# Performance work log

Hardware: AMD Instinct MI355X
Metric: run time of the kernel (lower is better)

The kernel has to match this reference:

```python
import jax, jax.numpy as jnp
import numpy as np
from jax import lax

H = 256          # hidden_size
VOCAB = 30000
N_OPS = 9
N_COLS = 16
T = 4            # num_time_steps
Q = 64           # question length
N_NUM = 8        # numbers appearing in the question
ROWS = 1_000_000

# operation indices (Neural Programmer, ICLR 2016 op set)
OP_SUM, OP_COUNT, OP_DIFF, OP_GREATER, OP_LESSER, OP_AND, OP_OR, OP_ASSIGN, OP_RESET = range(N_OPS)


def setup_inputs() -> dict:
    key = jax.random.key(0)
    ks = jax.random.split(key, 13)
    s = 0.05
    f32 = jnp.float32
    return {
        "input_question": jax.random.randint(ks[0], (Q,), 0, VOCAB),
        "input_question_numbers": jax.random.randint(ks[1], (N_NUM,), 0, 100),
        "left_word_indices": jax.random.randint(ks[2], (N_NUM,), 0, Q),
        "table": jax.random.normal(ks[3], (ROWS, N_COLS), f32),
        # learned parameters
        "emb": jax.random.normal(ks[4], (VOCAB, H), f32) * s,      # question word embeddings
        "Wx": jax.random.normal(ks[5], (H, H), f32) * s,           # question RNN input weight
        "Wh": jax.random.normal(ks[6], (H, H), f32) * s,           # question RNN recurrent weight
        "W_op": jax.random.normal(ks[7], (H, 2 * H), f32) * s,     # selector (op branch)
        "op_emb": jax.random.normal(ks[8], (N_OPS, H), f32) * s,   # operation embeddings
        "W_col": jax.random.normal(ks[9], (H, 2 * H), f32) * s,    # selector (column branch)
        "col_emb": jax.random.normal(ks[10], (N_COLS, H), f32) * s,# column embeddings
        "W_hist": jax.random.normal(ks[11], (H, 3 * H), f32) * s,  # history RNN
        "U": jax.random.normal(ks[12], (2, H), f32) * s,           # lesser/greater pivot vectors
    }


def reference(input_question, input_question_numbers, left_word_indices, table,
              emb, Wx, Wh, W_op, op_emb, W_col, col_emb, W_hist, U):
    dt = table.dtype
    hid = Wx.shape[0]

    # ---- question RNN (simple tanh RNN) ----
    xs = emb[input_question]                               # [Q, H]
    def step(h, x):
        h2 = jnp.tanh(x @ Wx.T + h @ Wh.T)
        return h2, h2
    q, hs = lax.scan(step, jnp.zeros((hid,), dt), xs)      # q=[H], hs=[Q,H]

    # ---- pivot computation (z_matrix = hidden states left of each number) ----
    z = hs[left_word_indices]                              # [N_NUM, H]
    nums = input_question_numbers.astype(dt)               # [N_NUM]
    l_pivot = jax.nn.softmax(z @ U[0]) @ nums              # scalar
    g_pivot = jax.nn.softmax(z @ U[1]) @ nums              # scalar

    # soft comparison maps (pivots are timestep-independent; compute once)
    sel_l = jax.nn.sigmoid(l_pivot - table)                # [R, C] ~ [table < l_pivot]
    sel_g = jax.nn.sigmoid(table - g_pivot)                # [R, C] ~ [table > g_pivot]

    h_hist = jnp.zeros((hid,), dt)
    scalars = [jnp.zeros((), dt)]
    rs_list = [jnp.ones((table.shape[0],), dt)]
    lookup = jnp.zeros(table.shape, dt)

    for _ in range(T):
        rs1 = rs_list[-1]
        rs2 = rs_list[max(0, len(rs_list) - 2)]
        s1 = scalars[-1]
        s3 = scalars[max(0, len(scalars) - 3)]

        # selector: soft op / column distributions from [question; history]
        qh = jnp.concatenate([q, h_hist])                  # [2H]
        a_op = jax.nn.softmax(op_emb @ jnp.tanh(W_op @ qh))    # [N_OPS]
        a_col = jax.nn.softmax(col_emb @ jnp.tanh(W_col @ qh)) # [N_COLS]

        # row select (soft mixture over ops)
        rs = (a_op[OP_GREATER] * (sel_g @ a_col)
              + a_op[OP_LESSER] * (sel_l @ a_col)
              + a_op[OP_AND] * jnp.minimum(rs1, rs2)
              + a_op[OP_OR] * jnp.maximum(rs1, rs2)
              + a_op[OP_RESET] * jnp.ones_like(rs1)
              + (a_op[OP_SUM] + a_op[OP_COUNT] + a_op[OP_DIFF] + a_op[OP_ASSIGN]) * rs1)

        # scalar answer
        scalar = (a_op[OP_SUM] * jnp.sum(rs1 @ table)
                  + a_op[OP_COUNT] * jnp.sum(rs1)
                  + a_op[OP_DIFF] * (s3 - s1))

        # lookup answer: assign op prints selected rows/columns
        lookup = a_op[OP_ASSIGN] * rs[:, None] * a_col[None, :]

        # history RNN
        c = jnp.concatenate([a_op @ op_emb, a_col @ col_emb, h_hist])  # [3H]
        h_hist = jnp.tanh(W_hist @ c)

        rs_list.append(rs)
        scalars.append(scalar)

    return scalars[-1], lookup
```

## Files before the change

### kernel.cpp

```cpp
#include <hip/hip_runtime.h>
#include <hip/hip_fp16.h>
#include <math.h>

#define HDIM   256
#define QLEN   64
#define NNUM   8
#define NOPS   9
#define NCOLS  16
#define TSTEPS 4


#define WS_LPIV 0
#define WS_GPIV 1
#define WS_ACOL 2
#define WS_AOP  66
#define WS_Q    112
#define WS_PQO  368
#define WS_PQC  624
#define WS_HS   880
#define WS_XP   2928
#define WS_AH   19312
#define WS_BH   21616
#define WS_WH16 25712
#define WS_M16  58480
#define WS_PART 156784
#define NBLK_C  2048
#define PRE2_BLOCKS 409

typedef _Float16 f16x8 __attribute__((ext_vector_type(8)));
typedef _Float16 f16x4 __attribute__((ext_vector_type(4)));
typedef float    f32x4 __attribute__((ext_vector_type(4)));

__device__ __forceinline__ float fast_tanh(float x) {
    return 1.0f - 2.0f / (__expf(2.0f * x) + 1.0f);
}

__global__ void precompute_kernel(const int* __restrict__ q,
                                  const float* __restrict__ emb,
                                  const float* __restrict__ Wx,
                                  const float* __restrict__ Wh,
                                  float* __restrict__ ws) {
    int gid = blockIdx.x * 256 + threadIdx.x;
    if (gid < QLEN * HDIM) {
        int t = gid >> 8, j = gid & 255;
        const float4* x4 = (const float4*)(emb + (size_t)q[t] * HDIM);
        const float4* w4 = (const float4*)(Wx + (size_t)j * HDIM);
        float s = 0.f;
        for (int k = 0; k < HDIM / 4; k++) {
            float4 a = x4[k], b = w4[k];
            s += a.x * b.x + a.y * b.y + a.z * b.z + a.w * b.w;
        }
        ws[WS_XP + t * HDIM + j] = s;
    } else {
        int did = gid - QLEN * HDIM;
        int hidx = did * 2;
        int e = hidx & 7, qr = (hidx >> 3) & 15, quad = (hidx >> 7) & 3;
        int kk = (hidx >> 9) & 7, t = hidx >> 12;
        const float* src = Wh + (size_t)(16 * t + qr) * HDIM + kk * 32 + quad * 8 + e;
        float2 v = *(const float2*)src;
        ((__half2*)(ws + WS_WH16))[did] = __floats2half2_rn(v.x, v.y);
    }
}

__global__ __launch_bounds__(256, 1) void rnn_kernel(
        float* __restrict__ ws,
        const int* __restrict__ lwi,
        const float* __restrict__ W_op,
        const float* __restrict__ W_col,
        const float* __restrict__ W_hist,
        const float* __restrict__ op_emb,
        const float* __restrict__ col_emb,
        const float* __restrict__ table,
        int rows) {
    if (blockIdx.x >= 1 + PRE2_BLOCKS) {
        int wid = blockIdx.x - 1 - PRE2_BLOCKS;
        const f32x4* t4 = (const f32x4*)table;
        long n4 = (long)rows * (NCOLS / 4);
        f32x4 acc = {0.f, 0.f, 0.f, 0.f};
        for (long i = (long)wid * 256 + threadIdx.x; i < n4; i += (long)2048 * 256)
            acc += t4[i];
        asm volatile("" :: "v"(acc));
        return;
    }
    if (blockIdx.x != 0) {
        int gid = (blockIdx.x - 1) * 256 + threadIdx.x;
        if (gid < HDIM * NOPS) {
            int j = gid / NOPS, o = gid % NOPS;
            const float4* w4 = (const float4*)(W_hist + (size_t)j * (3 * HDIM));
            const float4* e4 = (const float4*)(op_emb + (size_t)o * HDIM);
            float s = 0.f;
            for (int k = 0; k < HDIM / 4; k++) {
                float4 a = w4[k], b = e4[k];
                s += a.x * b.x + a.y * b.y + a.z * b.z + a.w * b.w;
            }
            ws[WS_AH + gid] = s;
        } else if (gid < HDIM * NOPS + HDIM * NCOLS) {
            int idx = gid - HDIM * NOPS;
            int j = idx / NCOLS, c = idx % NCOLS;
            const float4* w4 = (const float4*)(W_hist + (size_t)j * (3 * HDIM) + HDIM);
            const float4* e4 = (const float4*)(col_emb + (size_t)c * HDIM);
            float s = 0.f;
            for (int k = 0; k < HDIM / 4; k++) {
                float4 a = w4[k], b = e4[k];
                s += a.x * b.x + a.y * b.y + a.z * b.z + a.w * b.w;
            }
            ws[WS_BH + idx] = s;
        } else if (gid < HDIM * NOPS + HDIM * NCOLS + 98304) {
            int did = gid - (HDIM * NOPS + HDIM * NCOLS);
            int mat = did >> 15;
            int hidx = (did & 32767) * 2;
            int e = hidx & 7, j = (hidx >> 3) & 255, i = hidx >> 11;
            const float* src;
            if (mat == 0)      src = W_op   + (size_t)j * (2 * HDIM) + HDIM     + i * 8 + e;
            else if (mat == 1) src = W_col  + (size_t)j * (2 * HDIM) + HDIM     + i * 8 + e;
            else               src = W_hist + (size_t)j * (3 * HDIM) + 2 * HDIM + i * 8 + e;
            float2 v = *(const float2*)src;
            ((__half2*)(ws + WS_M16))[did] = __floats2half2_rn(v.x, v.y);
        }
        return;
    }

    __shared__ float xpL[QLEN * HDIM];
    __shared__ _Float16 hF[2][HDIM];
    __shared__ unsigned stepmask[QLEN];

    const int tid = threadIdx.x;
    const int wave = tid >> 6, lane = tid & 63;
    const int quad = lane >> 4, qr = lane & 15;
    const int myrow = 64 * wave + 16 * (qr >> 2) + quad * 4 + (qr & 3);

    #pragma unroll
    for (int i = 0; i < 16; i++) {
        int idx = (i * 256 + tid) * 4;
        *(float4*)(xpL + idx) = *(const float4*)(ws + WS_XP + idx);
    }
    if (tid < QLEN) {
        unsigned m = 0;
        #pragma unroll
        for (int i = 0; i < NNUM; i++) m |= (lwi[i] == tid) ? (1u << i) : 0u;
        stepmask[tid] = m;
    }
    const _Float16* wsh = (const _Float16*)(ws + WS_WH16);
    f16x8 aW[4][8];
    #pragma unroll
    for (int r = 0; r < 4; r++)
        #pragma unroll
        for (int kk = 0; kk < 8; kk++)
            aW[r][kk] = *(const f16x8*)(wsh + ((size_t)(((4 * wave + r) * 8 + kk) * 64 + lane)) * 8);
    #pragma unroll
    for (int r = 0; r < 4; r++)
        #pragma unroll
        for (int kk = 0; kk < 8; kk++) {
            f32x4 t = __builtin_bit_cast(f32x4, aW[r][kk]);
            asm volatile("" : "+v"(t));
            aW[r][kk] = __builtin_bit_cast(f16x8, t);
        }
    hF[0][tid] = (_Float16)0.f;
    __syncthreads();

    for (int s = 0; s < QLEN; s++) {
        const _Float16* hb = hF[s & 1];
        f16x8 bfrag[8];
        #pragma unroll
        for (int kk = 0; kk < 8; kk++)
            bfrag[kk] = *(const f16x8*)(hb + kk * 32 + quad * 8);
        f32x4 acc[4], accB[4];
        #pragma unroll
        for (int r = 0; r < 4; r++) {
            acc[r]  = (f32x4){0.f, 0.f, 0.f, 0.f};
            accB[r] = (f32x4){0.f, 0.f, 0.f, 0.f};
        }
        #pragma unroll
        for (int kk = 0; kk < 4; kk++)
            #pragma unroll
            for (int r = 0; r < 4; r++)
                acc[r] = __builtin_amdgcn_mfma_f32_16x16x32_f16(aW[r][kk], bfrag[kk], acc[r], 0, 0, 0);
        #pragma unroll
        for (int kk = 4; kk < 8; kk++)
            #pragma unroll
            for (int r = 0; r < 4; r++)
                accB[r] = __builtin_amdgcn_mfma_f32_16x16x32_f16(aW[r][kk], bfrag[kk], accB[r], 0, 0, 0);
        #pragma unroll
        for (int r = 0; r < 4; r++) acc[r] += accB[r];

        f32x4 t01 = (qr & 4) ? acc[1] : acc[0];
        f32x4 t23 = (qr & 4) ? acc[3] : acc[2];
        f32x4 tt  = (qr & 8) ? t23 : t01;
        float e01 = (qr & 1) ? tt.y : tt.x;
        float e23 = (qr & 1) ? tt.w : tt.z;
        float v   = (qr & 2) ? e23 : e01;

        float h = fast_tanh(v + xpL[s * HDIM + myrow]);
        hF[(s + 1) & 1][myrow] = (_Float16)h;
        unsigned m = stepmask[s];
        while (m) {
            int i = __builtin_ctz(m);
            ws[WS_HS + i * HDIM + myrow] = h;
            m &= m - 1;
        }
        if (s == QLEN - 1) ws[WS_Q + myrow] = h;
        __syncthreads();
    }
}

__global__ void qproj_kernel(const float* __restrict__ W_op,
                             const float* __restrict__ W_col,
                             float* __restrict__ ws) {
    int gid = blockIdx.x * 256 + threadIdx.x;
    int dot = gid >> 5, l = gid & 31;
    int mat = dot >> 8, j = dot & 255;
    const float* w = (mat ? W_col : W_op) + (size_t)j * (2 * HDIM) + l * 8;
    const float* qv = ws + WS_Q + l * 8;
    float4 a0 = *(const float4*)w,        a1 = *(const float4*)(w + 4);
    float4 b0 = *(const float4*)qv,       b1 = *(const float4*)(qv + 4);
    float s = a0.x * b0.x + a0.y * b0.y + a0.z * b0.z + a0.w * b0.w
            + a1.x * b1.x + a1.y * b1.y + a1.z * b1.z + a1.w * b1.w;
    s += __shfl_xor(s, 1); s += __shfl_xor(s, 2); s += __shfl_xor(s, 4);
    s += __shfl_xor(s, 8); s += __shfl_xor(s, 16);
    if (l == 0) ws[(mat ? WS_PQC : WS_PQO) + j] = s;
}

__global__ __launch_bounds__(256) void select_kernel(
        float* __restrict__ ws,
        const float* __restrict__ U,
        const int* __restrict__ nums,
        const float* __restrict__ op_emb,
        const float* __restrict__ col_emb) {
    __shared__ float zu[16];
    __shared__ float hH[HDIM];
    __shared__ float top_op[HDIM], top_col[HDIM], mh[HDIM];
    __shared__ float logits[32];
    __shared__ float aop_s[NOPS], acol_s[NCOLS];

    const int tid = threadIdx.x;

    {
        int g = tid >> 4, l = tid & 15;
        int i = g >> 1, u = g & 1;
        const float* z = ws + WS_HS + i * HDIM + l * 16;
        const float* uu = U + u * HDIM + l * 16;
        float s = 0.f;
        #pragma unroll
        for (int k = 0; k < 4; k++) {
            float4 a = *(const float4*)(z + k * 4), b = *(const float4*)(uu + k * 4);
            s += a.x * b.x + a.y * b.y + a.z * b.z + a.w * b.w;
        }
        s += __shfl_xor(s, 1); s += __shfl_xor(s, 2);
        s += __shfl_xor(s, 4); s += __shfl_xor(s, 8);
        if (l == 0) zu[g] = s;
    }
    if (tid < HDIM) hH[tid] = 0.f;
    __syncthreads();
    if (tid == 0) {
        #pragma unroll
        for (int u = 0; u < 2; u++) {
            float mx = -1e30f;
            for (int i = 0; i < NNUM; i++) mx = fmaxf(mx, zu[i * 2 + u]);
            float se = 0.f, pv = 0.f;
            for (int i = 0; i < NNUM; i++) {
                float e = __expf(zu[i * 2 + u] - mx);
                se += e;
                pv += e * (float)nums[i];
            }
            ws[u] = pv / se;
        }
    }
    __syncthreads();

    const _Float16* wsm = (const _Float16*)(ws + WS_M16);
    const float pqo = ws[WS_PQO + tid];
    const float pqc = ws[WS_PQC + tid];

    for (int t = 0; t < TSTEPS; t++) {
        float so = 0.f, sc = 0.f, sh = 0.f;
        #pragma unroll
        for (int i = 0; i < 32; i++) {
            float4 h0 = *(const float4*)(hH + i * 8);
            float4 h1 = *(const float4*)(hH + i * 8 + 4);
            f16x8 a = *(const f16x8*)(wsm + ((size_t)(0 * 32 + i) * 256 + tid) * 8);
            f16x8 b = *(const f16x8*)(wsm + ((size_t)(1 * 32 + i) * 256 + tid) * 8);
            f16x8 c = *(const f16x8*)(wsm + ((size_t)(2 * 32 + i) * 256 + tid) * 8);
            so += (float)a[0]*h0.x + (float)a[1]*h0.y + (float)a[2]*h0.z + (float)a[3]*h0.w
                + (float)a[4]*h1.x + (float)a[5]*h1.y + (float)a[6]*h1.z + (float)a[7]*h1.w;
            sc += (float)b[0]*h0.x + (float)b[1]*h0.y + (float)b[2]*h0.z + (float)b[3]*h0.w
                + (float)b[4]*h1.x + (float)b[5]*h1.y + (float)b[6]*h1.z + (float)b[7]*h1.w;
            sh += (float)c[0]*h0.x + (float)c[1]*h0.y + (float)c[2]*h0.z + (float)c[3]*h0.w
                + (float)c[4]*h1.x + (float)c[5]*h1.y + (float)c[6]*h1.z + (float)c[7]*h1.w;
        }
        top_op[tid]  = fast_tanh(pqo + so);
        top_col[tid] = fast_tanh(pqc + sc);
        mh[tid] = sh;
        __syncthreads();

        #pragma unroll
        for (int d0 = 0; d0 < 32; d0 += 8) {
            int d = d0 + (tid >> 5), l = tid & 31;
            if (d < 25) {
                float s = 0.f;
                if (d < NOPS) {
                    const float* e = op_emb + (size_t)d * HDIM;
                    #pragma unroll
                    for (int m = 0; m < 8; m++) s += e[l * 8 + m] * top_op[l * 8 + m];
                } else {
                    const float* e = col_emb + (size_t)(d - NOPS) * HDIM;
                    #pragma unroll
                    for (int m = 0; m < 8; m++) s += e[l * 8 + m] * top_col[l * 8 + m];
                }
                s += __shfl_xor(s, 1); s += __shfl_xor(s, 2); s += __shfl_xor(s, 4);
                s += __shfl_xor(s, 8); s += __shfl_xor(s, 16);
                if (l == 0) logits[d] = s;
            }
        }
        __syncthreads();
        if (tid == 0) {
            float mx = -1e30f;
            for (int o = 0; o < NOPS; o++) mx = fmaxf(mx, logits[o]);
            float se = 0.f, e[NOPS];
            for (int o = 0; o < NOPS; o++) { e[o] = __expf(logits[o] - mx); se += e[o]; }
            for (int o = 0; o < NOPS; o++) {
                float a = e[o] / se;
                aop_s[o] = a;
                ws[WS_AOP + t * NOPS + o] = a;
            }
        } else if (tid == 32) {
            float mx = -1e30f;
            for (int c = 0; c < NCOLS; c++) mx = fmaxf(mx, logits[NOPS + c]);
            float se = 0.f, e[NCOLS];
            for (int c = 0; c < NCOLS; c++) { e[c] = __expf(logits[NOPS + c] - mx); se += e[c]; }
            for (int c = 0; c < NCOLS; c++) {
                float a = e[c] / se;
                acol_s[c] = a;
                ws[WS_ACOL + t * NCOLS + c] = a;
            }
        }
        __syncthreads();
        {
            float s = mh[tid];
            const float* ah = ws + WS_AH + tid * NOPS;
            #pragma unroll
            for (int o = 0; o < NOPS; o++) s += ah[o] * aop_s[o];
            const float* bh = ws + WS_BH + tid * NCOLS;
            #pragma unroll
            for (int c = 0; c < NCOLS; c++) s += bh[c] * acol_s[c];
            float hv = fast_tanh(s);
            __syncthreads();
            hH[tid] = hv;
        }
        __syncthreads();
    }
}

__global__ __launch_bounds__(256) void table_kernel(
        const float* __restrict__ table,
        const float* __restrict__ wsc,
        float* __restrict__ wspart,
        float* __restrict__ out,
        int rows) {
    const int tid = threadIdx.x;
    const int cq = tid & 3;
    const float lpiv = wsc[WS_LPIV];
    const float gpiv = wsc[WS_GPIV];
    float4 acol4[TSTEPS];
    float wg[TSTEPS], wl[TSTEPS], wand[TSTEPS], wor[TSTEPS], wrst[TSTEPS], wpass[TSTEPS];
    #pragma unroll
    for (int t = 0; t < TSTEPS; t++) {
        acol4[t] = make_float4(wsc[WS_ACOL + t * NCOLS + cq * 4 + 0],
                               wsc[WS_ACOL + t * NCOLS + cq * 4 + 1],
                               wsc[WS_ACOL + t * NCOLS + cq * 4 + 2],
                               wsc[WS_ACOL + t * NCOLS + cq * 4 + 3]);
        wg[t]   = wsc[WS_AOP + t * NOPS + 3];
        wl[t]   = wsc[WS_AOP + t * NOPS + 4];
        wand[t] = wsc[WS_AOP + t * NOPS + 5];
        wor[t]  = wsc[WS_AOP + t * NOPS + 6];
        wrst[t] = wsc[WS_AOP + t * NOPS + 8];
        wpass[t] = wsc[WS_AOP + t * NOPS + 0] + wsc[WS_AOP + t * NOPS + 1]
                 + wsc[WS_AOP + t * NOPS + 2] + wsc[WS_AOP + t * NOPS + 7];
    }
    const float wassign = wsc[WS_AOP + 3 * NOPS + 7];

    float dAcc[TSTEPS] = {0.f, 0.f, 0.f, 0.f};
    float nAcc[TSTEPS] = {0.f, 0.f, 0.f, 0.f};
    const long rowsL = rows;

    for (long r0 = (long)blockIdx.x * 64; r0 < rowsL; r0 += (long)NBLK_C * 64) {
        long row = r0 + (tid >> 2);
        bool valid = row < rowsL;
        f32x4 tv = {0.f, 0.f, 0.f, 0.f};
        if (valid)
            tv = *(const f32x4*)(table + row * NCOLS + cq * 4);
        float prs = tv.x + tv.y + tv.z + tv.w;
        float pg[4], pl[4];
        {
            float c0 = tv.x, c1 = tv.y, c2 = tv.z, c3 = tv.w;
            float sg0 = __builtin_amdgcn_rcpf(1.f + __expf(gpiv - c0));
            float sg1 = __builtin_amdgcn_rcpf(1.f + __expf(gpiv - c1));
            float sg2 = __builtin_amdgcn_rcpf(1.f + __expf(gpiv - c2));
            float sg3 = __builtin_amdgcn_rcpf(1.f + __expf(gpiv - c3));
            float sl0 = __builtin_amdgcn_rcpf(1.f + __expf(c0 - lpiv));
            float sl1 = __builtin_amdgcn_rcpf(1.f + __expf(c1 - lpiv));
            float sl2 = __builtin_amdgcn_rcpf(1.f + __expf(c2 - lpiv));
            float sl3 = __builtin_amdgcn_rcpf(1.f + __expf(c3 - lpiv));
            #pragma unroll
            for (int t = 0; t < TSTEPS; t++) {
                pg[t] = sg0 * acol4[t].x + sg1 * acol4[t].y + sg2 * acol4[t].z + sg3 * acol4[t].w;
                pl[t] = sl0 * acol4[t].x + sl1 * acol4[t].y + sl2 * acol4[t].z + sl3 * acol4[t].w;
            }
        }
        prs += __shfl_xor(prs, 1); prs += __shfl_xor(prs, 2);
        #pragma unroll
        for (int t = 0; t < TSTEPS; t++) {
            pg[t] += __shfl_xor(pg[t], 1); pg[t] += __shfl_xor(pg[t], 2);
            pl[t] += __shfl_xor(pl[t], 1); pl[t] += __shfl_xor(pl[t], 2);
        }
        float rs1 = 1.f, rs2 = 1.f;
        float vf = valid ? 1.f : 0.f;
        #pragma unroll
        for (int i = 0; i < TSTEPS; i++) {
            dAcc[i] += vf * rs1 * prs;
            nAcc[i] += vf * rs1;
            float nrs = wg[i] * pg[i] + wl[i] * pl[i]
                      + wand[i] * fminf(rs1, rs2) + wor[i] * fmaxf(rs1, rs2)
                      + wrst[i] + wpass[i] * rs1;
            rs2 = rs1;
            rs1 = nrs;
        }
        if (valid) {
            float wa = wassign * rs1;
            float* ob = out + 1 + row * NCOLS + cq * 4;
            ob[0] = wa * acol4[3].x;
            ob[1] = wa * acol4[3].y;
            ob[2] = wa * acol4[3].z;
            ob[3] = wa * acol4[3].w;
        }
    }

    #pragma unroll
    for (int i = 0; i < TSTEPS; i++) {
        #pragma unroll
        for (int off = 32; off >= 1; off >>= 1) {
            dAcc[i] += __shfl_xor(dAcc[i], off);
            nAcc[i] += __shfl_xor(nAcc[i], off);
        }
    }
    __shared__ float redl[4][8];
    int wv = tid >> 6, ln = tid & 63;
    if (ln == 0) {
        #pragma unroll
        for (int i = 0; i < TSTEPS; i++) {
            redl[wv][i] = dAcc[i];
            redl[wv][4 + i] = nAcc[i];
        }
    }
    __syncthreads();
    if (tid < 8) {
        float s = redl[0][tid] + redl[1][tid] + redl[2][tid] + redl[3][tid];
        wspart[blockIdx.x * 8 + tid] = 0.25f * s;
    }
}

__global__ void finalize_kernel(const float* __restrict__ ws, float* __restrict__ out) {
    __shared__ float red[8];
    int a = threadIdx.x >> 5, l = threadIdx.x & 31;
    float s = 0.f;
    for (int b = l; b < NBLK_C; b += 32) s += ws[WS_PART + b * 8 + a];
    s += __shfl_xor(s, 1, 32); s += __shfl_xor(s, 2, 32); s += __shfl_xor(s, 4, 32);
    s += __shfl_xor(s, 8, 32); s += __shfl_xor(s, 16, 32);
    if (l == 0) red[a] = s;
    __syncthreads();
    if (threadIdx.x == 0) {
        float Dv[4] = {red[0], red[1], red[2], red[3]};
        float Nv[4] = {red[4], red[5], red[6], red[7]};
        const float* aop = ws + WS_AOP;
        float sc[5];
        sc[0] = 0.f;
        #pragma unroll
        for (int i = 0; i < 4; i++) {
            float s1 = sc[i];
            float s3 = sc[(i >= 2) ? (i - 2) : 0];
            sc[i + 1] = aop[i * NOPS + 0] * Dv[i] + aop[i * NOPS + 1] * Nv[i]
                      + aop[i * NOPS + 2] * (s3 - s1);
        }
        out[0] = sc[4];
    }
}

extern "C" void kernel_launch(void* const* d_in, const int* in_sizes, int n_in,
                              void* d_out, int out_size, void* d_ws, size_t ws_size,
                              hipStream_t stream) {
    const int*   q       = (const int*)d_in[0];
    const int*   nums    = (const int*)d_in[1];
    const int*   lwi     = (const int*)d_in[2];
    const float* table   = (const float*)d_in[3];
    const float* emb     = (const float*)d_in[4];
    const float* Wx      = (const float*)d_in[5];
    const float* Wh      = (const float*)d_in[6];
    const float* W_op    = (const float*)d_in[7];
    const float* op_emb  = (const float*)d_in[8];
    const float* W_col   = (const float*)d_in[9];
    const float* col_emb = (const float*)d_in[10];
    const float* W_hist  = (const float*)d_in[11];
    const float* U       = (const float*)d_in[12];
    float* out = (float*)d_out;
    float* ws  = (float*)d_ws;
    int rows = in_sizes[3] / NCOLS;

    precompute_kernel<<<192, 256, 0, stream>>>(q, emb, Wx, Wh, ws);
    rnn_kernel<<<1 + PRE2_BLOCKS + 2048, 256, 0, stream>>>(
        ws, lwi, W_op, W_col, W_hist, op_emb, col_emb, table, rows);
    qproj_kernel<<<64, 256, 0, stream>>>(W_op, W_col, ws);
    select_kernel<<<1, 256, 0, stream>>>(ws, U, nums, op_emb, col_emb);
    table_kernel<<<NBLK_C, 256, 0, stream>>>(
        table, ws, ws + WS_PART, out, rows);
    finalize_kernel<<<1, 256, 0, stream>>>(ws, out);
}
```

Before: 260.6 us.

## Fuse question projection and selector into RNN block, move weight prep earlier

Moves the W_hist/op_emb/col_emb products and the fp16 weight repacking out of the RNN launch and into the precompute kernel. Folds the q-projection and the selector/history loop into block 0 of the RNN kernel, so two separate kernel launches disappear from the serial critical path. The cost is that the q-projection now runs in a single block, with each thread doing a strided 256-element dot product instead of spreading that work over 64 blocks. That could lengthen the serial chain while the table-prefetch blocks run alongside.

Measured after the change: 313.7 us. 1.2x slower.

```diff
diff --git a/kernel.cpp b/kernel.cpp
--- a/kernel.cpp
+++ b/kernel.cpp
@@ -15,8 +15,6 @@
 #define WS_ACOL 2
 #define WS_AOP  66
 #define WS_Q    112
-#define WS_PQO  368
-#define WS_PQC  624
 #define WS_HS   880
 #define WS_XP   2928
 #define WS_AH   19312
@@ -25,7 +23,6 @@
 #define WS_M16  58480
 #define WS_PART 156784
 #define NBLK_C  2048
-#define PRE2_BLOCKS 409
 
 typedef _Float16 f16x8 __attribute__((ext_vector_type(8)));
 typedef _Float16 f16x4 __attribute__((ext_vector_type(4)));
@@ -39,6 +36,11 @@
                                   const float* __restrict__ emb,
                                   const float* __restrict__ Wx,
                                   const float* __restrict__ Wh,
+                                  const float* __restrict__ W_op,
+                                  const float* __restrict__ W_col,
+                                  const float* __restrict__ W_hist,
+                                  const float* __restrict__ op_emb,
+                                  const float* __restrict__ col_emb,
                                   float* __restrict__ ws) {
     int gid = blockIdx.x * 256 + threadIdx.x;
     if (gid < QLEN * HDIM) {
@@ -51,7 +53,7 @@
             s += a.x * b.x + a.y * b.y + a.z * b.z + a.w * b.w;
         }
         ws[WS_XP + t * HDIM + j] = s;
-    } else {
+    } else if (gid < 49152) {
         int did = gid - QLEN * HDIM;
         int hidx = did * 2;
         int e = hidx & 7, qr = (hidx >> 3) & 15, quad = (hidx >> 7) & 3;
@@ -59,21 +61,55 @@
         const float* src = Wh + (size_t)(16 * t + qr) * HDIM + kk * 32 + quad * 8 + e;
         float2 v = *(const float2*)src;
         ((__half2*)(ws + WS_WH16))[did] = __floats2half2_rn(v.x, v.y);
-    }
-}
-
-__global__ __launch_bounds__(256, 1) void rnn_kernel(
+    } else if (gid < 49152 + HDIM * NOPS) {
+        int idx = gid - 49152;
+        int j = idx / NOPS, o = idx % NOPS;
+        const float4* w4 = (const float4*)(W_hist + (size_t)j * (3 * HDIM));
+        const float4* e4 = (const float4*)(op_emb + (size_t)o * HDIM);
+        float s = 0.f;
+        for (int k = 0; k < HDIM / 4; k++) {
+            float4 a = w4[k], b = e4[k];
+            s += a.x * b.x + a.y * b.y + a.z * b.z + a.w * b.w;
+        }
+        ws[WS_AH + idx] = s;
+    } else if (gid < 51456 + HDIM * NCOLS) {
+        int idx = gid - 51456;
+        int j = idx / NCOLS, c = idx % NCOLS;
+        const float4* w4 = (const float4*)(W_hist + (size_t)j * (3 * HDIM) + HDIM);
+        const float4* e4 = (const float4*)(col_emb + (size_t)c * HDIM);
+        float s = 0.f;
+        for (int k = 0; k < HDIM / 4; k++) {
+            float4 a = w4[k], b = e4[k];
+            s += a.x * b.x + a.y * b.y + a.z * b.z + a.w * b.w;
+        }
+        ws[WS_BH + idx] = s;
+    } else if (gid < 55552 + 98304) {
+        int did = gid - 55552;
+        int mat = did >> 15;
+        int hidx = (did & 32767) * 2;
+        int e = hidx & 7, j = (hidx >> 3) & 255, i = hidx >> 11;
+        const float* src;
+        if (mat == 0)      src = W_op   + (size_t)j * (2 * HDIM) + HDIM     + i * 8 + e;
+        else if (mat == 1) src = W_col  + (size_t)j * (2 * HDIM) + HDIM     + i * 8 + e;
+        else               src = W_hist + (size_t)j * (3 * HDIM) + 2 * HDIM + i * 8 + e;
+        float2 v = *(const float2*)src;
+        ((__half2*)(ws + WS_M16))[did] = __floats2half2_rn(v.x, v.y);
+    }
+}
+
+__global__ __launch_bounds__(256, 1) void mega_kernel(
         float* __restrict__ ws,
         const int* __restrict__ lwi,
         const float* __restrict__ W_op,
         const float* __restrict__ W_col,
-        const float* __restrict__ W_hist,
         const float* __restrict__ op_emb,
         const float* __restrict__ col_emb,
+        const float* __restrict__ U,
+        const int* __restrict__ nums,
         const float* __restrict__ table,
         int rows) {
-    if (blockIdx.x >= 1 + PRE2_BLOCKS) {
-        int wid = blockIdx.x - 1 - PRE2_BLOCKS;
+    if (blockIdx.x != 0) {
+        int wid = blockIdx.x - 1;
         const f32x4* t4 = (const f32x4*)table;
         long n4 = (long)rows * (NCOLS / 4);
         f32x4 acc = {0.f, 0.f, 0.f, 0.f};
@@ -82,43 +118,6 @@
         asm volatile("" :: "v"(acc));
         return;
     }
-    if (blockIdx.x != 0) {
-        int gid = (blockIdx.x - 1) * 256 + threadIdx.x;
-        if (gid < HDIM * NOPS) {
-            int j = gid / NOPS, o = gid % NOPS;
-            const float4* w4 = (const float4*)(W_hist + (size_t)j * (3 * HDIM));
-            const float4* e4 = (const float4*)(op_emb + (size_t)o * HDIM);
-            float s = 0.f;
-            for (int k = 0; k < HDIM / 4; k++) {
-                float4 a = w4[k], b = e4[k];
-                s += a.x * b.x + a.y * b.y + a.z * b.z + a.w * b.w;
-            }
-            ws[WS_AH + gid] = s;
-        } else if (gid < HDIM * NOPS + HDIM * NCOLS) {
-            int idx = gid - HDIM * NOPS;
-            int j = idx / NCOLS, c = idx % NCOLS;
-            const float4* w4 = (const float4*)(W_hist + (size_t)j * (3 * HDIM) + HDIM);
-            const float4* e4 = (const float4*)(col_emb + (size_t)c * HDIM);
-            float s = 0.f;
-            for (int k = 0; k < HDIM / 4; k++) {
-                float4 a = w4[k], b = e4[k];
-                s += a.x * b.x + a.y * b.y + a.z * b.z + a.w * b.w;
-            }
-            ws[WS_BH + idx] = s;
-        } else if (gid < HDIM * NOPS + HDIM * NCOLS + 98304) {
-            int did = gid - (HDIM * NOPS + HDIM * NCOLS);
-            int mat = did >> 15;
-            int hidx = (did & 32767) * 2;
-            int e = hidx & 7, j = (hidx >> 3) & 255, i = hidx >> 11;
-            const float* src;
-            if (mat == 0)      src = W_op   + (size_t)j * (2 * HDIM) + HDIM     + i * 8 + e;
-            else if (mat == 1) src = W_col  + (size_t)j * (2 * HDIM) + HDIM     + i * 8 + e;
-            else               src = W_hist + (size_t)j * (3 * HDIM) + 2 * HDIM + i * 8 + e;
-            float2 v = *(const float2*)src;
-            ((__half2*)(ws + WS_M16))[did] = __floats2half2_rn(v.x, v.y);
-        }
-        return;
-    }
 
     __shared__ float xpL[QLEN * HDIM];
     __shared__ _Float16 hF[2][HDIM];
@@ -201,38 +200,26 @@
         if (s == QLEN - 1) ws[WS_Q + myrow] = h;
         __syncthreads();
     }
-}
-
-__global__ void qproj_kernel(const float* __restrict__ W_op,
-                             const float* __restrict__ W_col,
-                             float* __restrict__ ws) {
-    int gid = blockIdx.x * 256 + threadIdx.x;
-    int dot = gid >> 5, l = gid & 31;
-    int mat = dot >> 8, j = dot & 255;
-    const float* w = (mat ? W_col : W_op) + (size_t)j * (2 * HDIM) + l * 8;
-    const float* qv = ws + WS_Q + l * 8;
-    float4 a0 = *(const float4*)w,        a1 = *(const float4*)(w + 4);
-    float4 b0 = *(const float4*)qv,       b1 = *(const float4*)(qv + 4);
-    float s = a0.x * b0.x + a0.y * b0.y + a0.z * b0.z + a0.w * b0.w
-            + a1.x * b1.x + a1.y * b1.y + a1.z * b1.z + a1.w * b1.w;
-    s += __shfl_xor(s, 1); s += __shfl_xor(s, 2); s += __shfl_xor(s, 4);
-    s += __shfl_xor(s, 8); s += __shfl_xor(s, 16);
-    if (l == 0) ws[(mat ? WS_PQC : WS_PQO) + j] = s;
-}
-
-__global__ __launch_bounds__(256) void select_kernel(
-        float* __restrict__ ws,
-        const float* __restrict__ U,
-        const int* __restrict__ nums,
-        const float* __restrict__ op_emb,
-        const float* __restrict__ col_emb) {
+
+    float pqo = 0.f, pqc = 0.f;
+    {
+        const float* qv = ws + WS_Q;
+        const float* wo = W_op  + (size_t)tid * (2 * HDIM);
+        const float* wc = W_col + (size_t)tid * (2 * HDIM);
+        for (int k = 0; k < HDIM; k += 4) {
+            float4 qq = *(const float4*)(qv + k);
+            float4 a  = *(const float4*)(wo + k);
+            float4 b  = *(const float4*)(wc + k);
+            pqo += a.x * qq.x + a.y * qq.y + a.z * qq.z + a.w * qq.w;
+            pqc += b.x * qq.x + b.y * qq.y + b.z * qq.z + b.w * qq.w;
+        }
+    }
+
     __shared__ float zu[16];
     __shared__ float hH[HDIM];
     __shared__ float top_op[HDIM], top_col[HDIM], mh[HDIM];
     __shared__ float logits[32];
     __shared__ float aop_s[NOPS], acol_s[NCOLS];
-
-    const int tid = threadIdx.x;
 
     {
         int g = tid >> 4, l = tid & 15;
@@ -249,7 +236,7 @@
         s += __shfl_xor(s, 4); s += __shfl_xor(s, 8);
         if (l == 0) zu[g] = s;
     }
-    if (tid < HDIM) hH[tid] = 0.f;
+    hH[tid] = 0.f;
     __syncthreads();
     if (tid == 0) {
         #pragma unroll
@@ -268,8 +255,6 @@
     __syncthreads();
 
     const _Float16* wsm = (const _Float16*)(ws + WS_M16);
-    const float pqo = ws[WS_PQO + tid];
-    const float pqc = ws[WS_PQC + tid];
 
     for (int t = 0; t < TSTEPS; t++) {
         float so = 0.f, sc = 0.f, sh = 0.f;
@@ -504,11 +489,10 @@
     float* ws  = (float*)d_ws;
     int rows = in_sizes[3] / NCOLS;
 
-    precompute_kernel<<<192, 256, 0, stream>>>(q, emb, Wx, Wh, ws);
-    rnn_kernel<<<1 + PRE2_BLOCKS + 2048, 256, 0, stream>>>(
-        ws, lwi, W_op, W_col, W_hist, op_emb, col_emb, table, rows);
-    qproj_kernel<<<64, 256, 0, stream>>>(W_op, W_col, ws);
-    select_kernel<<<1, 256, 0, stream>>>(ws, U, nums, op_emb, col_emb);
+    precompute_kernel<<<601, 256, 0, stream>>>(
+        q, emb, Wx, Wh, W_op, W_col, W_hist, op_emb, col_emb, ws);
+    mega_kernel<<<1 + 2048, 256, 0, stream>>>(
+        ws, lwi, W_op, W_col, op_emb, col_emb, U, nums, table, rows);
     table_kernel<<<NBLK_C, 256, 0, stream>>>(
         table, ws, ws + WS_PART, out, rows);
     finalize_kernel<<<1, 256, 0, stream>>>(ws, out);
```
